# Optimization experiments

Hardware: AMD Instinct MI355X
Metric: run time of the kernel (lower is better)

Reference implementation:

```python
import jax, jax.numpy as jnp
import numpy as np

N_STATE = 1024
N_HEAD = 16
B, S = 2, 2048
NEG = -1e9  # finite stand-in for -inf in the additive causal mask


def setup_inputs() -> dict:
    key = jax.random.key(0)
    ks = jax.random.split(key, 8)
    sd = N_STATE ** -0.5
    x = jax.random.normal(ks[0], (B, S, N_STATE), dtype=jnp.float32)
    # additive causal mask, as in Whisper: upper triangle = -inf
    i = jnp.arange(S)
    mask = jnp.where(i[None, :] > i[:, None], NEG, 0.0).astype(jnp.float32)
    return {
        "x": x,
        "mask": mask,
        "Wq": jax.random.normal(ks[1], (N_STATE, N_STATE), jnp.float32) * sd,
        "bq": jax.random.normal(ks[2], (N_STATE,), jnp.float32) * 0.02,
        "Wk": jax.random.normal(ks[3], (N_STATE, N_STATE), jnp.float32) * sd,
        "Wv": jax.random.normal(ks[4], (N_STATE, N_STATE), jnp.float32) * sd,
        "bv": jax.random.normal(ks[5], (N_STATE,), jnp.float32) * 0.02,
        "Wo": jax.random.normal(ks[6], (N_STATE, N_STATE), jnp.float32) * sd,
        "bo": jax.random.normal(ks[7], (N_STATE,), jnp.float32) * 0.02,
    }


def reference(x, mask, Wq, bq, Wk, Wv, bv, Wo, bo):
    B_, S_, D = x.shape
    H = N_HEAD
    hd = D // H
    scale = hd ** -0.25  # applied to both q and k, per the source

    q = (x @ Wq + bq).reshape(B_, S_, H, hd) * scale   # [B,S,H,hd]
    k = (x @ Wk).reshape(B_, S_, H, hd) * scale        # key has no bias
    v = (x @ Wv + bv).reshape(B_, S_, H, hd)

    qk = jnp.einsum("bqhd,bkhd->bhqk", q, k) + mask[:S_, :S_]
    w = jax.nn.softmax(qk.astype(jnp.float32), axis=-1).astype(q.dtype)
    o = jnp.einsum("bhqk,bkhd->bqhd", w, v).reshape(B_, S_, D)
    return o @ Wo + bo
```

## Files before the change

kernel.cpp:

```cpp
#include <hip/hip_runtime.h>
#include <hip/hip_bf16.h>

#define BB 2
#define SS 2048
#define DD 1024
#define HH 16
#define HD 64
#define QKSCALE 0.35355339059327373f
#define QKSCALE_E2 0.42466090144f
#define NEGBIG (-1e9f)

using u16 = unsigned short;
typedef __attribute__((ext_vector_type(8))) short short8;
typedef __attribute__((ext_vector_type(4))) float floatx4;
typedef __attribute__((ext_vector_type(4))) unsigned short ushort4v;

#define GLOBAL_AS __attribute__((address_space(1)))
#define LDS_AS __attribute__((address_space(3)))

__device__ __forceinline__ u16 f2b(float f) {
  union { float f; unsigned u; } v; v.f = f;
  return (u16)((v.u + 0x7fffu + ((v.u >> 16) & 1u)) >> 16);
}

__device__ __forceinline__ u16 bconv(float f) {
  union { __hip_bfloat16 h; u16 u; } cv;
  cv.h = __float2bfloat16(f);
  return cv.u;
}

__device__ __forceinline__ float ex2(float f) {
  return __builtin_amdgcn_exp2f(f);
}

__device__ __forceinline__ floatx4 vmax4(floatx4 a, floatx4 b) {
  return (floatx4){fmaxf(a[0], b[0]), fmaxf(a[1], b[1]),
                   fmaxf(a[2], b[2]), fmaxf(a[3], b[3])};
}

__device__ __forceinline__ void gload_lds16(const void* g, void* l) {
  __builtin_amdgcn_global_load_lds((GLOBAL_AS void*)(g), (LDS_AS void*)(l), 16, 0, 0);
}

__global__ __launch_bounds__(256) void cvt_bf16x4(const float4* __restrict__ src,
                                                  ushort4v* __restrict__ dst, int n4) {
  int i = blockIdx.x * 256 + threadIdx.x;
  if (i >= n4) return;
  float4 f = src[i];
  ushort4v o = { f2b(f.x), f2b(f.y), f2b(f.z), f2b(f.w) };
  dst[i] = o;
}

__global__ __launch_bounds__(256) void transpose_w(const float* __restrict__ s0,
                                                   const float* __restrict__ s1,
                                                   const float* __restrict__ s2,
                                                   const float* __restrict__ s3,
                                                   u16* __restrict__ dst) {
  __shared__ float tile[32][33];
  const float* src = (blockIdx.z == 0) ? s0 : (blockIdx.z == 1) ? s1
                   : (blockIdx.z == 2) ? s2 : s3;
  u16* d = dst + (size_t)blockIdx.z * 1024 * 1024;
  int c0 = blockIdx.x * 32, r0 = blockIdx.y * 32;
  int tx = threadIdx.x, ty = threadIdx.y;
#pragma unroll
  for (int i = 0; i < 4; ++i)
    tile[ty + i * 8][tx] = src[(size_t)(r0 + ty + i * 8) * 1024 + c0 + tx];
  __syncthreads();
#pragma unroll
  for (int i = 0; i < 4; ++i)
    d[(size_t)(c0 + ty + i * 8) * 1024 + r0 + tx] = f2b(tile[tx][ty + i * 8]);
}

__global__ __launch_bounds__(256) void transpose_v(const u16* __restrict__ v,
                                                   u16* __restrict__ vtd) {
  __shared__ u16 tile[32][34];
  int b = blockIdx.z;
  int c0 = blockIdx.x * 32;
  int s0 = blockIdx.y * 32;
  int tx = threadIdx.x, ty = threadIdx.y;
#pragma unroll
  for (int i = 0; i < 4; ++i)
    tile[ty + i * 8][tx] = v[(size_t)(b * SS + s0 + ty + i * 8) * DD + c0 + tx];
  __syncthreads();
#pragma unroll
  for (int i = 0; i < 4; ++i)
    vtd[(size_t)(b * DD + c0 + ty + i * 8) * SS + s0 + tx] = tile[tx][ty + i * 8];
}

template <typename OutT>
__global__ __launch_bounds__(256)
void gemm_bt(const u16* __restrict__ A, const u16* __restrict__ Bt,
             OutT* __restrict__ C, const float* __restrict__ bias,
             float scale, int M, int N, int K) {
  const int tid = threadIdx.x;
  const int lane = tid & 63;
  const int w = tid >> 6;
  const int m0 = blockIdx.x * 128;
  const int n0 = blockIdx.y * 128;
  __shared__ u16 As[128 * 64];
  __shared__ u16 Bs[128 * 64];
  floatx4 acc[4][4];
#pragma unroll
  for (int i = 0; i < 4; ++i)
#pragma unroll
    for (int j = 0; j < 4; ++j) acc[i][j] = (floatx4){0.f, 0.f, 0.f, 0.f};

  const int wr = (w >> 1) * 64;
  const int wc = (w & 1) * 64;
  const int g = lane >> 4;
  const int lr = lane & 15;
  const size_t strideA = (size_t)K * 2;

  for (int k0 = 0; k0 < K; k0 += 64) {
#pragma unroll
    for (int p = 0; p < 4; ++p) {
      int L = tid * 16 + p * 4096;
      int row = L >> 7;
      int cb = (L ^ ((row & 7) << 4)) & 127;
      gload_lds16((const char*)A + (size_t)(m0 + row) * strideA + k0 * 2 + cb,
                  (char*)As + p * 4096 + w * 1024);
      gload_lds16((const char*)Bt + (size_t)(n0 + row) * strideA + k0 * 2 + cb,
                  (char*)Bs + p * 4096 + w * 1024);
    }
    __syncthreads();
#pragma unroll
    for (int ks = 0; ks < 2; ++ks) {
      short8 af[4], bf[4];
      const int c0 = ks * 32 + g * 8;
#pragma unroll
      for (int mi = 0; mi < 4; ++mi) {
        int row = wr + mi * 16 + lr;
        af[mi] = *(const short8*)(As + row * 64 + (c0 ^ ((row & 7) << 3)));
      }
#pragma unroll
      for (int ni = 0; ni < 4; ++ni) {
        int row = wc + ni * 16 + lr;
        bf[ni] = *(const short8*)(Bs + row * 64 + (c0 ^ ((row & 7) << 3)));
      }
#pragma unroll
      for (int mi = 0; mi < 4; ++mi)
#pragma unroll
        for (int ni = 0; ni < 4; ++ni)
          acc[mi][ni] = __builtin_amdgcn_mfma_f32_16x16x32_bf16(af[mi], bf[ni],
                                                                acc[mi][ni], 0, 0, 0);
    }
    __syncthreads();
  }
#pragma unroll
  for (int ni = 0; ni < 4; ++ni) {
    int col = n0 + wc + ni * 16 + lr;
    float bvv = bias ? bias[col] : 0.f;
#pragma unroll
    for (int mi = 0; mi < 4; ++mi) {
#pragma unroll
      for (int r = 0; r < 4; ++r) {
        int rowg = m0 + wr + mi * 16 + g * 4 + r;
        float val = (acc[mi][ni][r] + bvv) * scale;
        if constexpr (sizeof(OutT) == 4) C[(size_t)rowg * N + col] = val;
        else C[(size_t)rowg * N + col] = (OutT)f2b(val);
      }
    }
  }
}

__global__ __launch_bounds__(256)
void gemm_qkv(const u16* __restrict__ A, const u16* __restrict__ Wt3,
              u16* __restrict__ Out3, const float* __restrict__ bq,
              const float* __restrict__ bv) {
  const int seg = blockIdx.z;
  const u16* Bt = Wt3 + (size_t)seg * 1024 * 1024;
  u16* C = Out3 + (size_t)seg * 4096 * 1024;
  const float* bias = (seg == 0) ? bq : (seg == 2) ? bv : nullptr;
  const float scale = (seg == 2) ? 1.0f : QKSCALE_E2;

  const int tid = threadIdx.x;
  const int lane = tid & 63;
  const int w = tid >> 6;
  const int m0 = blockIdx.x * 128;
  const int n0 = blockIdx.y * 128;
  __shared__ u16 As[128 * 64];
  __shared__ u16 Bs[128 * 64];
  floatx4 acc[4][4];
#pragma unroll
  for (int i = 0; i < 4; ++i)
#pragma unroll
    for (int j = 0; j < 4; ++j) acc[i][j] = (floatx4){0.f, 0.f, 0.f, 0.f};
  const int wr = (w >> 1) * 64;
  const int wc = (w & 1) * 64;
  const int g = lane >> 4;
  const int lr = lane & 15;
  const size_t strideA = (size_t)1024 * 2;

  for (int k0 = 0; k0 < 1024; k0 += 64) {
#pragma unroll
    for (int p = 0; p < 4; ++p) {
      int L = tid * 16 + p * 4096;
      int row = L >> 7;
      int cb = (L ^ ((row & 7) << 4)) & 127;
      gload_lds16((const char*)A + (size_t)(m0 + row) * strideA + k0 * 2 + cb,
                  (char*)As + p * 4096 + w * 1024);
      gload_lds16((const char*)Bt + (size_t)(n0 + row) * strideA + k0 * 2 + cb,
                  (char*)Bs + p * 4096 + w * 1024);
    }
    __syncthreads();
#pragma unroll
    for (int ks = 0; ks < 2; ++ks) {
      short8 af[4], bf[4];
      const int c0 = ks * 32 + g * 8;
#pragma unroll
      for (int mi = 0; mi < 4; ++mi) {
        int row = wr + mi * 16 + lr;
        af[mi] = *(const short8*)(As + row * 64 + (c0 ^ ((row & 7) << 3)));
      }
#pragma unroll
      for (int ni = 0; ni < 4; ++ni) {
        int row = wc + ni * 16 + lr;
        bf[ni] = *(const short8*)(Bs + row * 64 + (c0 ^ ((row & 7) << 3)));
      }
#pragma unroll
      for (int mi = 0; mi < 4; ++mi)
#pragma unroll
        for (int ni = 0; ni < 4; ++ni)
          acc[mi][ni] = __builtin_amdgcn_mfma_f32_16x16x32_bf16(af[mi], bf[ni],
                                                                acc[mi][ni], 0, 0, 0);
    }
    __syncthreads();
  }
#pragma unroll
  for (int ni = 0; ni < 4; ++ni) {
    int col = n0 + wc + ni * 16 + lr;
    float bvv = bias ? bias[col] : 0.f;
#pragma unroll
    for (int mi = 0; mi < 4; ++mi) {
#pragma unroll
      for (int r = 0; r < 4; ++r) {
        int rowg = m0 + wr + mi * 16 + g * 4 + r;
        C[(size_t)rowg * 1024 + col] = f2b((acc[mi][ni][r] + bvv) * scale);
      }
    }
  }
}

__device__ __forceinline__ void stream_softmax(floatx4 (&sa)[4], float& m, float& l,
                                               floatx4 (&acc)[4], u16* pl,
                                               bool diag, int wlr, int g, int lr) {
  if (diag) {
#pragma unroll
    for (int ct = 0; ct < 4; ++ct)
#pragma unroll
      for (int r = 0; r < 4; ++r)
        if (ct * 16 + g * 4 + r > wlr) sa[ct][r] += NEGBIG;
  }
  floatx4 v = vmax4(vmax4(sa[0], sa[1]), vmax4(sa[2], sa[3]));
  float mx = fmaxf(fmaxf(v[0], v[1]), fmaxf(v[2], v[3]));
  mx = fmaxf(mx, __shfl_xor(mx, 16, 64));
  mx = fmaxf(mx, __shfl_xor(mx, 32, 64));
  if (!__all(mx <= m + 8.f)) {
    float mn = fmaxf(m, mx);
    float al = ex2(m - mn);
    l *= al;
#pragma unroll
    for (int dt = 0; dt < 4; ++dt) acc[dt] *= al;
    m = mn;
  }
  floatx4 p[4];
#pragma unroll
  for (int ct = 0; ct < 4; ++ct)
#pragma unroll
    for (int r = 0; r < 4; ++r)
      p[ct][r] = ex2(sa[ct][r] - m);
  floatx4 s = (p[0] + p[1]) + (p[2] + p[3]);
  float rs = (s[0] + s[1]) + (s[2] + s[3]);
  rs += __shfl_xor(rs, 16, 64);
  rs += __shfl_xor(rs, 32, 64);
  l += rs;
#pragma unroll
  for (int ct = 0; ct < 4; ++ct) {
    ushort4v pk = { bconv(p[ct][0]), bconv(p[ct][1]),
                    bconv(p[ct][2]), bconv(p[ct][3]) };
    *(ushort4v*)((char*)pl + ((lr * 128 + ct * 32 + g * 8) ^ ((lr & 7) << 4))) = pk;
  }
}

__global__ __launch_bounds__(256, 4)
void flash_attn(const u16* __restrict__ q, const u16* __restrict__ k,
                const u16* __restrict__ vt, u16* __restrict__ o) {
  const int tid = threadIdx.x;
  const int lane = tid & 63;
  const int w = tid >> 6;
  const int g = lane >> 4;
  const int lr = lane & 15;
  const int i = (int)blockIdx.x;
  const int x = i & 7;
  const int kk = i >> 3;
  const int c = kk & 31;
  const int quarter = kk >> 5;
  const int gg = x + 8 * quarter;
  const int b = gg >> 4;
  const int h = gg & 15;
  int qt;
  if (quarter == 0) qt = 31 - c;
  else if (quarter == 1) qt = c;
  else if (quarter == 2) qt = (47 - c) & 31;
  else qt = (c + 16) & 31;
  const int row0 = qt * 64 + w * 16;
  const int wlr = w * 16 + lr;

  __shared__ u16 Ks[2][64 * 64];
  __shared__ u16 Vs[2][64 * 64];
  __shared__ u16 Pl[4][16 * 64];

  short8 qf[2];
  {
    const u16* qp = q + (size_t)(b * SS + row0 + lr) * DD + h * HD + g * 8;
    qf[0] = *(const short8*)qp;
    qf[1] = *(const short8*)(qp + 32);
  }
  floatx4 acc[4];
#pragma unroll
  for (int dt = 0; dt < 4; ++dt) acc[dt] = (floatx4){0.f, 0.f, 0.f, 0.f};
  float m = -1e30f, l = 0.f;

  const char* kbase = (const char*)(k + (size_t)(b * SS) * DD + h * HD);
  const char* vbase = (const char*)(vt + (size_t)((b * HH + h) * HD) * SS);
  const int nt = qt + 1;

  auto stage = [&](int t, int buf) {
    const int kvb = t * 64;
#pragma unroll
    for (int p = 0; p < 2; ++p) {
      int L = tid * 16 + p * 4096;
      int row = L >> 7;
      int cb = (L ^ ((row & 7) << 4)) & 127;
      gload_lds16(kbase + (size_t)(kvb + row) * (DD * 2) + cb,
                  (char*)Ks + buf * 8192 + p * 4096 + w * 1024);
      gload_lds16(vbase + (size_t)row * (SS * 2) + kvb * 2 + cb,
                  (char*)Vs + buf * 8192 + p * 4096 + w * 1024);
    }
  };

  stage(0, 0);
  int cur = 0;
  for (int t = 0; t < nt; ++t) {
    __syncthreads();
    if (t + 1 < nt) stage(t + 1, cur ^ 1);
    const u16* kc = Ks[cur];
    const u16* vc = Vs[cur];

    floatx4 sa[4];
#pragma unroll
    for (int ct = 0; ct < 4; ++ct) sa[ct] = (floatx4){0.f, 0.f, 0.f, 0.f};
    __builtin_amdgcn_s_setprio(1);
#pragma unroll
    for (int ks = 0; ks < 2; ++ks) {
      const int c0 = ks * 32 + g * 8;
#pragma unroll
      for (int ct = 0; ct < 4; ++ct) {
        int row = ct * 16 + lr;
        short8 kf = *(const short8*)(kc + row * 64 + (c0 ^ ((row & 7) << 3)));
        sa[ct] = __builtin_amdgcn_mfma_f32_16x16x32_bf16(kf, qf[ks], sa[ct], 0, 0, 0);
      }
    }
    __builtin_amdgcn_s_setprio(0);

    stream_softmax(sa, m, l, acc, Pl[w], t == qt, wlr, g, lr);
    asm volatile("" ::: "memory");

    __builtin_amdgcn_s_setprio(1);
#pragma unroll
    for (int ks = 0; ks < 2; ++ks) {
      const int c0 = ks * 32 + g * 8;
      int pby = (lr * 128 + ks * 64 + g * 16) ^ ((lr & 7) << 4);
      short8 pf = *(const short8*)((const char*)Pl[w] + pby);
#pragma unroll
      for (int dt = 0; dt < 4; ++dt) {
        int row = dt * 16 + lr;
        short8 vf = *(const short8*)(vc + row * 64 + (c0 ^ ((row & 7) << 3)));
        acc[dt] = __builtin_amdgcn_mfma_f32_16x16x32_bf16(vf, pf, acc[dt], 0, 0, 0);
      }
    }
    __builtin_amdgcn_s_setprio(0);
    asm volatile("" ::: "memory");
    cur ^= 1;
  }

  float inv = 1.0f / l;
#pragma unroll
  for (int dt = 0; dt < 4; ++dt) {
    ushort4v pa = { bconv(acc[dt][0] * inv), bconv(acc[dt][1] * inv),
                    bconv(acc[dt][2] * inv), bconv(acc[dt][3] * inv) };
    *(ushort4v*)(o + (size_t)(b * SS + row0 + lr) * DD + h * HD + dt * 16 + g * 4) = pa;
  }
}

extern "C" void kernel_launch(void* const* d_in, const int* in_sizes, int n_in,
                              void* d_out, int out_size, void* d_ws, size_t ws_size,
                              hipStream_t stream) {
  const float* x  = (const float*)d_in[0];
  const float* Wq = (const float*)d_in[2];
  const float* bq = (const float*)d_in[3];
  const float* Wk = (const float*)d_in[4];
  const float* Wv = (const float*)d_in[5];
  const float* bv = (const float*)d_in[6];
  const float* Wo = (const float*)d_in[7];
  const float* bo = (const float*)d_in[8];
  float* out = (float*)d_out;

  char* ws = (char*)d_ws;
  u16* xb  = (u16*)(ws);
  u16* wt  = (u16*)(ws + (8u << 20));
  u16* qkv = (u16*)(ws + (16u << 20));
  u16* vb  = qkv + 2u * 4096 * 1024;
  u16* vtb = (u16*)(ws + (40u << 20));
  u16* ob  = (u16*)(ws + (48u << 20));
  u16* wot = wt + 3u * 1024 * 1024;

  dim3 tb(32, 8);
  cvt_bf16x4<<<4096, 256, 0, stream>>>((const float4*)x, (ushort4v*)xb,
                                       (BB * SS * DD) / 4);
  transpose_w<<<dim3(32, 32, 4), tb, 0, stream>>>(Wq, Wk, Wv, Wo, wt);
  gemm_qkv<<<dim3(32, 8, 3), 256, 0, stream>>>(xb, wt, qkv, bq, bv);
  transpose_v<<<dim3(32, 64, 2), tb, 0, stream>>>(vb, vtb);
  flash_attn<<<1024, 256, 0, stream>>>(qkv, qkv + (size_t)4096 * 1024, vtb, ob);
  gemm_bt<float><<<dim3(32, 8), 256, 0, stream>>>(ob, wot, out, bo, 1.0f,
                                                  4096, 1024, 1024);
}
```

Measured before the change: 128.0 us.

## Rewrite QKV GEMM as 256x256-tile, 8-wave, double-buffered pipelined kernel

Replaces the 128x128-tile, 4-wave QKV projection GEMM with a 256x256-tile kernel using 8 waves and double-buffered LDS. Each K step is split into four quadrant phases, and the next tile's halves are loaded asynchronously while MFMAs run, with explicit vmcnt waits and barriers. It also adds a block-index swizzle for L2 locality and raises MFMA priority with setprio. The aim is to hide global-load latency and improve data reuse, at the cost of more LDS and register pressure and fragile hand-counted wait values.

```diff
diff --git a/kernel.cpp b/kernel.cpp
--- a/kernel.cpp
+++ b/kernel.cpp
@@ -163,79 +163,139 @@
   }
 }
 
-__global__ __launch_bounds__(256)
-void gemm_qkv(const u16* __restrict__ A, const u16* __restrict__ Wt3,
-              u16* __restrict__ Out3, const float* __restrict__ bq,
-              const float* __restrict__ bv) {
-  const int seg = blockIdx.z;
-  const u16* Bt = Wt3 + (size_t)seg * 1024 * 1024;
-  u16* C = Out3 + (size_t)seg * 4096 * 1024;
-  const float* bias = (seg == 0) ? bq : (seg == 2) ? bv : nullptr;
-  const float scale = (seg == 2) ? 1.0f : QKSCALE_E2;
-
+template <int Q>
+__device__ __forceinline__ void qkv_phase_core(
+    const u16* __restrict__ Ah, const u16* __restrict__ Bh,
+    floatx4 (&acc)[4][4][2], int wsr, int wsc, int g, int lr) {
+  short8 af[4][2], bfv[2][2];
+#pragma unroll
+  for (int mi = 0; mi < 4; ++mi) {
+    int row = wsr * 64 + mi * 16 + lr;
+    int sw = (row & 7) << 4;
+#pragma unroll
+    for (int ks = 0; ks < 2; ++ks)
+      af[mi][ks] = *(const short8*)((const char*)Ah + row * 128 + ((ks * 64 + g * 16) ^ sw));
+  }
+#pragma unroll
+  for (int ni = 0; ni < 2; ++ni) {
+    int row = wsc * 32 + ni * 16 + lr;
+    int sw = (row & 7) << 4;
+#pragma unroll
+    for (int ks = 0; ks < 2; ++ks)
+      bfv[ni][ks] = *(const short8*)((const char*)Bh + row * 128 + ((ks * 64 + g * 16) ^ sw));
+  }
+  __builtin_amdgcn_s_setprio(1);
+#pragma unroll
+  for (int mi = 0; mi < 4; ++mi)
+#pragma unroll
+    for (int ni = 0; ni < 2; ++ni)
+#pragma unroll
+      for (int ks = 0; ks < 2; ++ks)
+        acc[Q][mi][ni] = __builtin_amdgcn_mfma_f32_16x16x32_bf16(
+            af[mi][ks], bfv[ni][ks], acc[Q][mi][ni], 0, 0, 0);
+  __builtin_amdgcn_s_setprio(0);
+}
+
+#define PH_WAIT(N)                                         \
+  do {                                                     \
+    asm volatile("s_waitcnt vmcnt(" #N ")" ::: "memory");  \
+    __builtin_amdgcn_s_barrier();                          \
+    __builtin_amdgcn_sched_barrier(0);                     \
+  } while (0)
+
+__global__ __launch_bounds__(512, 2)
+void gemm_qkv8(const u16* __restrict__ A, const u16* __restrict__ Wt3,
+               u16* __restrict__ Out3, const float* __restrict__ bq,
+               const float* __restrict__ bv) {
   const int tid = threadIdx.x;
   const int lane = tid & 63;
   const int w = tid >> 6;
-  const int m0 = blockIdx.x * 128;
-  const int n0 = blockIdx.y * 128;
-  __shared__ u16 As[128 * 64];
-  __shared__ u16 Bs[128 * 64];
-  floatx4 acc[4][4];
-#pragma unroll
-  for (int i = 0; i < 4; ++i)
-#pragma unroll
-    for (int j = 0; j < 4; ++j) acc[i][j] = (floatx4){0.f, 0.f, 0.f, 0.f};
-  const int wr = (w >> 1) * 64;
-  const int wc = (w & 1) * 64;
   const int g = lane >> 4;
   const int lr = lane & 15;
-  const size_t strideA = (size_t)1024 * 2;
-
-  for (int k0 = 0; k0 < 1024; k0 += 64) {
-#pragma unroll
-    for (int p = 0; p < 4; ++p) {
-      int L = tid * 16 + p * 4096;
+  const int wsr = w >> 2;
+  const int wsc = w & 3;
+  const int id = (int)blockIdx.x;
+  const int swz = (id & 7) * 24 + (id >> 3);
+  const int m0 = (swz & 15) * 256;
+  const int n0 = (swz >> 4) * 256;
+
+  __shared__ u16 Alds[2][2][128 * 64];
+  __shared__ u16 Blds[2][2][128 * 64];
+
+  const char* asrc = (const char*)A + (size_t)m0 * 2048;
+  const char* bsrc = (const char*)Wt3 + (size_t)n0 * 2048;
+
+  auto stage = [&](int mat, int kt, int half, int buf) {
+    const char* src = (mat == 0) ? asrc : bsrc;
+    char* dst = (char*)((mat == 0) ? &Alds[buf][half][0] : &Blds[buf][half][0]) + w * 1024;
+#pragma unroll
+    for (int j = 0; j < 2; ++j) {
+      int L = tid * 16 + j * 8192;
       int row = L >> 7;
       int cb = (L ^ ((row & 7) << 4)) & 127;
-      gload_lds16((const char*)A + (size_t)(m0 + row) * strideA + k0 * 2 + cb,
-                  (char*)As + p * 4096 + w * 1024);
-      gload_lds16((const char*)Bt + (size_t)(n0 + row) * strideA + k0 * 2 + cb,
-                  (char*)Bs + p * 4096 + w * 1024);
-    }
-    __syncthreads();
-#pragma unroll
-    for (int ks = 0; ks < 2; ++ks) {
-      short8 af[4], bf[4];
-      const int c0 = ks * 32 + g * 8;
+      gload_lds16(src + (size_t)(half * 128 + row) * 2048 + kt * 128 + cb,
+                  dst + j * 8192);
+    }
+  };
+
+  floatx4 acc[4][4][2];
+#pragma unroll
+  for (int q = 0; q < 4; ++q)
+#pragma unroll
+    for (int mi = 0; mi < 4; ++mi)
+#pragma unroll
+      for (int ni = 0; ni < 2; ++ni) acc[q][mi][ni] = (floatx4){0.f, 0.f, 0.f, 0.f};
+
+  stage(0, 0, 0, 0); stage(1, 0, 0, 0);
+  stage(0, 0, 1, 0); stage(1, 0, 1, 0);
+  stage(0, 1, 0, 1); stage(1, 1, 0, 1);
+
+  for (int kt = 0; kt < 15; ++kt) {
+    const int buf = kt & 1, nbuf = buf ^ 1;
+    PH_WAIT(6);
+    stage(0, kt + 1, 1, nbuf);
+    qkv_phase_core<0>(Alds[buf][0], Blds[buf][0], acc, wsr, wsc, g, lr);
+    PH_WAIT(6);
+    stage(1, kt + 1, 1, nbuf);
+    qkv_phase_core<1>(Alds[buf][0], Blds[buf][1], acc, wsr, wsc, g, lr);
+    PH_WAIT(6);
+    if (kt < 14) stage(0, kt + 2, 0, buf);
+    qkv_phase_core<2>(Alds[buf][1], Blds[buf][0], acc, wsr, wsc, g, lr);
+    PH_WAIT(6);
+    if (kt < 14) stage(1, kt + 2, 0, buf);
+    qkv_phase_core<3>(Alds[buf][1], Blds[buf][1], acc, wsr, wsc, g, lr);
+  }
+  {
+    PH_WAIT(4);
+    qkv_phase_core<0>(Alds[1][0], Blds[1][0], acc, wsr, wsc, g, lr);
+    PH_WAIT(0);
+    qkv_phase_core<1>(Alds[1][0], Blds[1][1], acc, wsr, wsc, g, lr);
+    __builtin_amdgcn_s_barrier();
+    qkv_phase_core<2>(Alds[1][1], Blds[1][0], acc, wsr, wsc, g, lr);
+    __builtin_amdgcn_s_barrier();
+    qkv_phase_core<3>(Alds[1][1], Blds[1][1], acc, wsr, wsc, g, lr);
+  }
+
+  const int seg = n0 >> 10;
+  const float scale = (seg == 2) ? 1.0f : QKSCALE_E2;
+  const float* bias = (seg == 0) ? bq : (seg == 2) ? bv : nullptr;
+  u16* outBase = Out3 + (size_t)seg * 4096 * 1024;
+  const int nnBase = n0 & 1023;
+#pragma unroll
+  for (int q = 0; q < 4; ++q) {
+    const int rq = (q >> 1) * 128, cq = (q & 1) * 128;
+#pragma unroll
+    for (int ni = 0; ni < 2; ++ni) {
+      int colInB = cq + wsc * 32 + ni * 16 + lr;
+      float bvv = bias ? bias[nnBase + colInB] : 0.f;
 #pragma unroll
       for (int mi = 0; mi < 4; ++mi) {
-        int row = wr + mi * 16 + lr;
-        af[mi] = *(const short8*)(As + row * 64 + (c0 ^ ((row & 7) << 3)));
-      }
-#pragma unroll
-      for (int ni = 0; ni < 4; ++ni) {
-        int row = wc + ni * 16 + lr;
-        bf[ni] = *(const short8*)(Bs + row * 64 + (c0 ^ ((row & 7) << 3)));
-      }
-#pragma unroll
-      for (int mi = 0; mi < 4; ++mi)
-#pragma unroll
-        for (int ni = 0; ni < 4; ++ni)
-          acc[mi][ni] = __builtin_amdgcn_mfma_f32_16x16x32_bf16(af[mi], bf[ni],
-                                                                acc[mi][ni], 0, 0, 0);
-    }
-    __syncthreads();
-  }
-#pragma unroll
-  for (int ni = 0; ni < 4; ++ni) {
-    int col = n0 + wc + ni * 16 + lr;
-    float bvv = bias ? bias[col] : 0.f;
-#pragma unroll
-    for (int mi = 0; mi < 4; ++mi) {
-#pragma unroll
-      for (int r = 0; r < 4; ++r) {
-        int rowg = m0 + wr + mi * 16 + g * 4 + r;
-        C[(size_t)rowg * 1024 + col] = f2b((acc[mi][ni][r] + bvv) * scale);
+#pragma unroll
+        for (int r = 0; r < 4; ++r) {
+          int rowg = m0 + rq + wsr * 64 + mi * 16 + g * 4 + r;
+          outBase[(size_t)rowg * 1024 + nnBase + colInB] =
+              f2b((acc[q][mi][ni][r] + bvv) * scale);
+        }
       }
     }
   }
@@ -419,7 +479,7 @@
   cvt_bf16x4<<<4096, 256, 0, stream>>>((const float4*)x, (ushort4v*)xb,
                                        (BB * SS * DD) / 4);
   transpose_w<<<dim3(32, 32, 4), tb, 0, stream>>>(Wq, Wk, Wv, Wo, wt);
-  gemm_qkv<<<dim3(32, 8, 3), 256, 0, stream>>>(xb, wt, qkv, bq, bv);
+  gemm_qkv8<<<192, 512, 0, stream>>>(xb, wt, qkv, bq, bv);
   transpose_v<<<dim3(32, 64, 2), tb, 0, stream>>>(vb, vtb);
   flash_attn<<<1024, 256, 0, stream>>>(qkv, qkv + (size_t)4096 * 1024, vtb, ob);
   gemm_bt<float><<<dim3(32, 8), 256, 0, stream>>>(ob, wot, out, bo, 1.0f,
```

Measured after the change: 133.8 us. +4.5%, slower.

## Double-buffer LDS tiles in projection GEMMs to overlap loads with MFMA

Applied to the files above, without the earlier changes.

Both projection GEMM kernels now use two LDS buffers per operand. The next K-tile is issued into the alternate buffer right after the barrier, before the MFMAs on the current tile run, and the trailing barrier is removed. This hides global-to-LDS latency behind compute. The change also raises wave priority around the MFMA block and adds a min-blocks-per-SM launch bound of 2. LDS per block doubles to 64KB, which may limit occupancy. Removing the trailing barrier relies on the single leading barrier to order reuse of each buffer.

```diff
diff --git a/kernel.cpp b/kernel.cpp
--- a/kernel.cpp
+++ b/kernel.cpp
@@ -88,7 +88,7 @@
 }
 
 template <typename OutT>
-__global__ __launch_bounds__(256)
+__global__ __launch_bounds__(256, 2)
 void gemm_bt(const u16* __restrict__ A, const u16* __restrict__ Bt,
              OutT* __restrict__ C, const float* __restrict__ bias,
              float scale, int M, int N, int K) {
@@ -97,8 +97,8 @@
   const int w = tid >> 6;
   const int m0 = blockIdx.x * 128;
   const int n0 = blockIdx.y * 128;
-  __shared__ u16 As[128 * 64];
-  __shared__ u16 Bs[128 * 64];
+  __shared__ u16 As[2][128 * 64];
+  __shared__ u16 Bs[2][128 * 64];
   floatx4 acc[4][4];
 #pragma unroll
   for (int i = 0; i < 4; ++i)
@@ -111,18 +111,27 @@
   const int lr = lane & 15;
   const size_t strideA = (size_t)K * 2;
 
-  for (int k0 = 0; k0 < K; k0 += 64) {
+  auto stage = [&](int k0, int buf) {
 #pragma unroll
     for (int p = 0; p < 4; ++p) {
       int L = tid * 16 + p * 4096;
       int row = L >> 7;
       int cb = (L ^ ((row & 7) << 4)) & 127;
       gload_lds16((const char*)A + (size_t)(m0 + row) * strideA + k0 * 2 + cb,
-                  (char*)As + p * 4096 + w * 1024);
+                  (char*)As[buf] + p * 4096 + w * 1024);
       gload_lds16((const char*)Bt + (size_t)(n0 + row) * strideA + k0 * 2 + cb,
-                  (char*)Bs + p * 4096 + w * 1024);
-    }
+                  (char*)Bs[buf] + p * 4096 + w * 1024);
+    }
+  };
+
+  const int nsteps = K >> 6;
+  stage(0, 0);
+  for (int t = 0; t < nsteps; ++t) {
+    const int buf = t & 1;
     __syncthreads();
+    if (t + 1 < nsteps) stage((t + 1) << 6, buf ^ 1);
+    const u16* as = As[buf];
+    const u16* bs = Bs[buf];
 #pragma unroll
     for (int ks = 0; ks < 2; ++ks) {
       short8 af[4], bf[4];
@@ -130,21 +139,22 @@
 #pragma unroll
       for (int mi = 0; mi < 4; ++mi) {
         int row = wr + mi * 16 + lr;
-        af[mi] = *(const short8*)(As + row * 64 + (c0 ^ ((row & 7) << 3)));
+        af[mi] = *(const short8*)(as + row * 64 + (c0 ^ ((row & 7) << 3)));
       }
 #pragma unroll
       for (int ni = 0; ni < 4; ++ni) {
         int row = wc + ni * 16 + lr;
-        bf[ni] = *(const short8*)(Bs + row * 64 + (c0 ^ ((row & 7) << 3)));
-      }
+        bf[ni] = *(const short8*)(bs + row * 64 + (c0 ^ ((row & 7) << 3)));
+      }
+      __builtin_amdgcn_s_setprio(1);
 #pragma unroll
       for (int mi = 0; mi < 4; ++mi)
 #pragma unroll
         for (int ni = 0; ni < 4; ++ni)
           acc[mi][ni] = __builtin_amdgcn_mfma_f32_16x16x32_bf16(af[mi], bf[ni],
                                                                 acc[mi][ni], 0, 0, 0);
-    }
-    __syncthreads();
+      __builtin_amdgcn_s_setprio(0);
+    }
   }
 #pragma unroll
   for (int ni = 0; ni < 4; ++ni) {
@@ -163,7 +173,7 @@
   }
 }
 
-__global__ __launch_bounds__(256)
+__global__ __launch_bounds__(256, 2)
 void gemm_qkv(const u16* __restrict__ A, const u16* __restrict__ Wt3,
               u16* __restrict__ Out3, const float* __restrict__ bq,
               const float* __restrict__ bv) {
@@ -178,8 +188,8 @@
   const int w = tid >> 6;
   const int m0 = blockIdx.x * 128;
   const int n0 = blockIdx.y * 128;
-  __shared__ u16 As[128 * 64];
-  __shared__ u16 Bs[128 * 64];
+  __shared__ u16 As[2][128 * 64];
+  __shared__ u16 Bs[2][128 * 64];
   floatx4 acc[4][4];
 #pragma unroll
   for (int i = 0; i < 4; ++i)
@@ -189,20 +199,27 @@
   const int wc = (w & 1) * 64;
   const int g = lane >> 4;
   const int lr = lane & 15;
-  const size_t strideA = (size_t)1024 * 2;
-
-  for (int k0 = 0; k0 < 1024; k0 += 64) {
+
+  auto stage = [&](int k0, int buf) {
 #pragma unroll
     for (int p = 0; p < 4; ++p) {
       int L = tid * 16 + p * 4096;
       int row = L >> 7;
       int cb = (L ^ ((row & 7) << 4)) & 127;
-      gload_lds16((const char*)A + (size_t)(m0 + row) * strideA + k0 * 2 + cb,
-                  (char*)As + p * 4096 + w * 1024);
-      gload_lds16((const char*)Bt + (size_t)(n0 + row) * strideA + k0 * 2 + cb,
-                  (char*)Bs + p * 4096 + w * 1024);
-    }
+      gload_lds16((const char*)A + (size_t)(m0 + row) * 2048 + k0 * 2 + cb,
+                  (char*)As[buf] + p * 4096 + w * 1024);
+      gload_lds16((const char*)Bt + (size_t)(n0 + row) * 2048 + k0 * 2 + cb,
+                  (char*)Bs[buf] + p * 4096 + w * 1024);
+    }
+  };
+
+  stage(0, 0);
+  for (int t = 0; t < 16; ++t) {
+    const int buf = t & 1;
     __syncthreads();
+    if (t + 1 < 16) stage((t + 1) << 6, buf ^ 1);
+    const u16* as = As[buf];
+    const u16* bs = Bs[buf];
 #pragma unroll
     for (int ks = 0; ks < 2; ++ks) {
       short8 af[4], bf[4];
@@ -210,21 +227,22 @@
 #pragma unroll
       for (int mi = 0; mi < 4; ++mi) {
         int row = wr + mi * 16 + lr;
-        af[mi] = *(const short8*)(As + row * 64 + (c0 ^ ((row & 7) << 3)));
+        af[mi] = *(const short8*)(as + row * 64 + (c0 ^ ((row & 7) << 3)));
       }
 #pragma unroll
       for (int ni = 0; ni < 4; ++ni) {
         int row = wc + ni * 16 + lr;
-        bf[ni] = *(const short8*)(Bs + row * 64 + (c0 ^ ((row & 7) << 3)));
-      }
+        bf[ni] = *(const short8*)(bs + row * 64 + (c0 ^ ((row & 7) << 3)));
+      }
+      __builtin_amdgcn_s_setprio(1);
 #pragma unroll
       for (int mi = 0; mi < 4; ++mi)
 #pragma unroll
         for (int ni = 0; ni < 4; ++ni)
           acc[mi][ni] = __builtin_amdgcn_mfma_f32_16x16x32_bf16(af[mi], bf[ni],
                                                                 acc[mi][ni], 0, 0, 0);
-    }
-    __syncthreads();
+      __builtin_amdgcn_s_setprio(0);
+    }
   }
 #pragma unroll
   for (int ni = 0; ni < 4; ++ni) {
```

After: 121.6 us. 1.05x faster.
